# Kernel optimization log

Measured on AMD Instinct MI355X. Metric: run time of the kernel, lower is better.

## Reference

```python
import jax, jax.numpy as jnp
import numpy as np

FS = 16            # fixStride
LAST_RATIO = 0.5
TAUA, TAUB = 10.0, 0.1
TOT_EPOCHS = 100
EPS = 1e-20
SEED = 777


def _safe_norm(diff):
    # ||diff||_2 with subgradient 0 at 0 (matches torch.norm backward at 0)
    sq = jnp.sum(diff * diff, axis=-1)
    d = jnp.sqrt(jnp.where(sq > 0, sq, 1.0))
    return jnp.where(sq > 0, d, 0.0)


def _forward(x, w_score, b_score, att_params, num_graphs, epoch):
    BN, C = x.shape
    B = int(num_graphs)
    N = BN // B
    RES = N - FS + 1                       # rows per graph (unfold1d)
    MAXP = int(np.ceil(N * LAST_RATIO))    # max_pivot_count = ceil(N*last_ratio/init_ratio)

    # --- TopKPool scorer (init_ratio==1.0): permute nodes per graph by desc score
    scores = (x @ w_score + b_score) / jnp.sqrt(jnp.sum(w_score ** 2))
    perm = jnp.argsort(-scores.reshape(B, N), axis=-1, stable=True)      # [B,N]
    xg = jnp.take_along_axis(x.reshape(B, N, C), perm[..., None], axis=1)

    # --- sliding-window edges: row r -> dests r..r+FS-1, src node r
    dst = jnp.arange(RES)[:, None] + jnp.arange(FS)[None, :]             # [RES,FS]
    x_src = xg[:, :RES, :]                                               # [B,RES,C]
    x_dst = xg[:, dst, :]                                                # [B,RES,FS,C]

    # getSM_ei + scatter_softmax over rows: att = [x_s, x_d] @ att_params
    a1, a2 = att_params[:C], att_params[C:]
    sm = jax.nn.softmax((xg @ a1)[:, :RES, None] + (xg @ a2)[:, dst], axis=-1)  # [B,RES,FS]

    # getDM_ei (sigma=1): gaussian-kernel edge distances
    gk = jnp.exp(-_safe_norm(x_src[:, :, None, :] - x_dst) / 2.0) - EPS  # [B,RES,FS]

    # scatterSort: stable descending sort of gk per row
    order = jnp.argsort(-gk, axis=-1, stable=True)
    gk_sort = jnp.take_along_axis(gk, order, axis=-1)
    sm_sort = jnp.take_along_axis(sm, order, axis=-1)

    # per-rank column logits: scatter-sum of sorted attention over rows of each graph
    logits = jnp.broadcast_to(sm_sort.sum(axis=1)[:, None, :], (B, RES, FS))
    logits = logits.at[:, :, 0].set(-jnp.inf)            # mask rank-0 (self edge)

    # gumbel-softmax with annealed temperature
    tau0 = TAUA * (TAUB / TAUA) ** (float(epoch) / TOT_EPOCHS)
    g = jax.random.gumbel(jax.random.key(SEED), (B, RES, FS), jnp.float32)
    gmb = jax.nn.softmax((g + logits) / tau0, axis=-1)

    # per-row threshold and shifted distances (unsorted layout)
    ths = jnp.sum(gk_sort * gmb, axis=-1, keepdims=True)
    shifted = jax.nn.relu(gk - ths)                      # [B,RES,FS]

    # scatter_min over positions 1..FS-1 (position 0 excluded via index redirect)
    delta = (jnp.argmin(shifted[:, :, 1:], axis=-1) + 1).astype(jnp.int32)  # [B,RES]

    # innerLoopStar: follow skip pointers from row 0, up to MAXP pivots
    def chain(delta_g):
        def step(ptr, _):
            valid = ptr < RES
            piv = jnp.where(valid, ptr, -1)
            nxt = jnp.where(valid, ptr + delta_g[jnp.clip(ptr, 0, RES - 1)], jnp.int32(RES))
            return nxt, piv
        _, pivs = jax.lax.scan(step, jnp.int32(0), None, length=MAXP)
        return pivs

    pivots = jax.vmap(chain)(delta)                      # [B,MAXP], -1 padded
    mask = pivots >= 0
    pooled = jnp.take_along_axis(xg, jnp.clip(pivots, 0, N - 1)[..., None], axis=1)
    pooled = pooled * mask[..., None]                    # [B,MAXP,C]
    return pooled, shifted, pivots


def setup_inputs() -> dict:
    key = jax.random.key(0)
    k0, k1, k2, k3 = jax.random.split(key, 4)
    B, N, C = 128, 512, 64
    return {
        "x": jax.random.normal(k0, (B * N, C), jnp.float32),
        "w_score": jax.random.normal(k1, (C,), jnp.float32),
        "b_score": jax.random.normal(k2, (), jnp.float32),
        "att_params": jax.random.normal(k3, (2 * C,), jnp.float32),
        "num_graphs": B,
        "epoch": 10,
    }


def reference(x, w_score, b_score, att_params, num_graphs, epoch):
    return _forward(x, w_score, b_score, att_params, num_graphs, epoch)
```

## Files before the change

### kernel.cpp

```cpp
#include <hip/hip_runtime.h>
#include <math.h>

#define BB 128
#define NN 512
#define CC 64
#define FS 16
#define RES 497
#define MAXP 256
#define BN (BB*NN)
#define GT (BB*RES*FS)
#define WPB 16
#define NCH 32
#define ROWS (WPB+FS-1)
#define PITCH 66
#define GW2 64
#define GBLK 8

__device__ __forceinline__ unsigned rotl32(unsigned x, int d){ return (x<<d)|(x>>(32-d)); }

__device__ __forceinline__ void threefry777(unsigned x0, unsigned x1, unsigned &o0, unsigned &o1){
  const unsigned ks0 = 0u, ks1 = 777u;
  const unsigned ks2 = 0x1BD11BDAu ^ ks0 ^ ks1;
  x0 += ks0; x1 += ks1;
  x0+=x1; x1=rotl32(x1,13); x1^=x0;
  x0+=x1; x1=rotl32(x1,15); x1^=x0;
  x0+=x1; x1=rotl32(x1,26); x1^=x0;
  x0+=x1; x1=rotl32(x1, 6); x1^=x0;
  x0+=ks1; x1+=ks2+1u;
  x0+=x1; x1=rotl32(x1,17); x1^=x0;
  x0+=x1; x1=rotl32(x1,29); x1^=x0;
  x0+=x1; x1=rotl32(x1,16); x1^=x0;
  x0+=x1; x1=rotl32(x1,24); x1^=x0;
  x0+=ks2; x1+=ks0+2u;
  x0+=x1; x1=rotl32(x1,13); x1^=x0;
  x0+=x1; x1=rotl32(x1,15); x1^=x0;
  x0+=x1; x1=rotl32(x1,26); x1^=x0;
  x0+=x1; x1=rotl32(x1, 6); x1^=x0;
  x0+=ks0; x1+=ks1+3u;
  x0+=x1; x1=rotl32(x1,17); x1^=x0;
  x0+=x1; x1=rotl32(x1,29); x1^=x0;
  x0+=x1; x1=rotl32(x1,16); x1^=x0;
  x0+=x1; x1=rotl32(x1,24); x1^=x0;
  x0+=ks1; x1+=ks2+4u;
  x0+=x1; x1=rotl32(x1,13); x1^=x0;
  x0+=x1; x1=rotl32(x1,15); x1^=x0;
  x0+=x1; x1=rotl32(x1,26); x1^=x0;
  x0+=x1; x1=rotl32(x1, 6); x1^=x0;
  x0+=ks2; x1+=ks0+5u;
  o0 = x0; o1 = x1;
}

__device__ __forceinline__ float gumbel_at_f32(unsigned p){
  unsigned o0, o1;
  threefry777(0u, p, o0, o1);
  unsigned bits = o0 ^ o1;
  float fl = __uint_as_float((bits >> 9) | 0x3f800000u) - 1.0f;
  float u  = fmaxf(1.17549435e-38f, fl);
  return -logf(-logf(u));
}

__device__ __forceinline__ double wave_push_f64(double v, int dstLane){
  int lo = __double2loint(v), hi = __double2hiint(v);
  int plo = __builtin_amdgcn_ds_permute(dstLane<<2, lo);
  int phi = __builtin_amdgcn_ds_permute(dstLane<<2, hi);
  return __hiloint2double(phi, plo);
}

__global__ __launch_bounds__(NN) void k_scoresort(const float* __restrict__ x,
    const float* __restrict__ w, const float* __restrict__ bsc,
    const float* __restrict__ att, double* __restrict__ s1s,
    double* __restrict__ s2s, int* __restrict__ perm){
  int b = blockIdx.x, t = threadIdx.x;
  __shared__ double ss[NN];
  __shared__ int    si[NN];
  __shared__ double l1[NN], l2[NN];

  double wn=0.0, dw=0.0, d1=0.0, d2=0.0;
  #pragma unroll
  for (int c=0;c<CC;c++){ double wv=(double)w[c]; wn += wv*wv; }
  const float4* xr = (const float4*)(x + (size_t)(b*NN+t)*CC);
  #pragma unroll
  for (int q=0;q<CC/4;q++){
    float4 v = xr[q];
    double xv;
    xv=(double)v.x; dw+=xv*(double)w[4*q+0]; d1+=xv*(double)att[4*q+0]; d2+=xv*(double)att[CC+4*q+0];
    xv=(double)v.y; dw+=xv*(double)w[4*q+1]; d1+=xv*(double)att[4*q+1]; d2+=xv*(double)att[CC+4*q+1];
    xv=(double)v.z; dw+=xv*(double)w[4*q+2]; d1+=xv*(double)att[4*q+2]; d2+=xv*(double)att[CC+4*q+2];
    xv=(double)v.w; dw+=xv*(double)w[4*q+3]; d1+=xv*(double)att[4*q+3]; d2+=xv*(double)att[CC+4*q+3];
  }
  double s = (dw + (double)bsc[0]) / sqrt(wn);
  int idx = t;
  l1[t] = d1;
  l2[t] = d2;

  for (int k = 2; k <= NN; k <<= 1){
    bool up = ((t & k) == 0);
    for (int j = k >> 1; j >= 64; j >>= 1){
      ss[t] = s; si[t] = idx;
      __syncthreads();
      double os = ss[t ^ j]; int oi = si[t ^ j];
      bool first = ((t & j) == 0);
      bool cmp = (s > os) || (s == os && idx < oi);
      bool keep = (cmp == (first == up));
      if (!keep){ s = os; idx = oi; }
      __syncthreads();
    }
    #pragma unroll
    for (int j = 32; j > 0; j >>= 1){
      if (j <= (k >> 1)){
        double os = __shfl_xor(s, j, 64);
        int    oi = __shfl_xor(idx, j, 64);
        bool first = ((t & j) == 0);
        bool cmp = (s > os) || (s == os && idx < oi);
        bool keep = (cmp == (first == up));
        if (!keep){ s = os; idx = oi; }
      }
    }
  }
  __syncthreads();
  perm[b*NN + t] = idx;
  s1s[b*NN + t] = l1[idx];
  s2s[b*NN + t] = l2[idx];
}

__global__ __launch_bounds__(256) void k_passA(const float* __restrict__ x,
    const int* __restrict__ perm, const double* __restrict__ s1s,
    const double* __restrict__ s2s, double* __restrict__ gkd,
    unsigned char* __restrict__ rank8, double* __restrict__ partial){
  int b = blockIdx.y, ch = blockIdx.x, tid = threadIdx.x;
  int i0 = ch*WPB;
  int nwin  = min(WPB, RES - i0);
  int nrows = min(ROWS, NN - i0);
  __shared__ float  xs[ROWS*PITCH];
  __shared__ int    pg[ROWS];
  __shared__ double wred[4][FS];

  if (tid < nrows) pg[tid] = perm[b*NN + i0 + tid];
  __syncthreads();
  for (int u = tid; u < nrows*16; u += 256){
    int r = u >> 4, seg = u & 15;
    float4 v = ((const float4*)(x + (size_t)(b*NN + pg[r])*CC))[seg];
    float2* dst = (float2*)&xs[r*PITCH + seg*4];
    dst[0] = make_float2(v.x, v.y);
    dst[1] = make_float2(v.z, v.w);
  }
  __syncthreads();

  int w = tid >> 4, j = tid & 15;
  int lane = tid & 63, gbase = lane & 48, wv = tid >> 6;
  bool act = (w < nwin);
  int i = i0 + w;

  double sq = 0.0;
  const float* rs = &xs[w*PITCH];
  const float* rd = &xs[(w+j)*PITCH];
  #pragma unroll
  for (int c2=0;c2<CC/2;c2++){
    float2 a  = *(const float2*)&rs[2*c2];
    float2 bb = *(const float2*)&rd[2*c2];
    double d0 = (double)a.x - (double)bb.x;
    double d1v= (double)a.y - (double)bb.y;
    sq += d0*d0;
    sq += d1v*d1v;
  }
  double d   = (sq > 0.0) ? sqrt(sq) : 0.0;
  double gkv = exp(-d*0.5) - 1e-20;

  int drow = min(i + j, NN-1);
  double smt = s1s[b*NN + i] + s2s[b*NN + drow];
  double m = smt;
  #pragma unroll
  for (int off=8; off; off>>=1) m = fmax(m, __shfl_xor(m, off, 16));
  double em = exp(smt - m);
  double ssum = em;
  #pragma unroll
  for (int off=8; off; off>>=1) ssum += __shfl_xor(ssum, off, 16);
  double smn = em / ssum;

  int rank = 0;
  #pragma unroll
  for (int k=0;k<16;k++){
    double gkk = __shfl(gkv, gbase + k, 64);
    rank += ((gkk > gkv) || (gkk == gkv && k < j)) ? 1 : 0;
  }

  if (act){
    size_t base = ((size_t)b*RES + i)*FS;
    gkd[base + j]   = gkv;
    rank8[base + j] = (unsigned char)rank;
  }

  double contrib = act ? smn : 0.0;
  double srt = wave_push_f64(contrib, gbase + rank);
  srt += __shfl_xor(srt, 16, 64);
  srt += __shfl_xor(srt, 32, 64);
  if (lane < FS) wred[wv][lane] = srt;
  __syncthreads();
  if (tid < FS){
    partial[((size_t)b*NCH + ch)*FS + tid] =
        wred[0][tid] + wred[1][tid] + wred[2][tid] + wred[3][tid];
  }
}

__global__ __launch_bounds__(GW2) void k_g_rng(double* __restrict__ dummy){
  int b = blockIdx.y;
  int win = blockIdx.x*GW2 + threadIdx.x;
  if (win >= RES) return;
  size_t base = ((size_t)b*RES + win)*FS;
  double m = -(double)INFINITY;
  #pragma unroll 2
  for (int s=1;s<FS;s++){
    double g = (double)gumbel_at_f32((unsigned)(base + (unsigned)s));
    m = fmax(m, g);
  }
  dummy[b*RES + win] = m;
}

__global__ __launch_bounds__(GW2) void k_gumbel(const double* __restrict__ gkd,
    const unsigned char* __restrict__ rank8, const double* __restrict__ partial,
    const int* __restrict__ epoch_p, float* __restrict__ shifted_out,
    int* __restrict__ delta){
  int b = blockIdx.y, tid = threadIdx.x;
  int win = blockIdx.x*GW2 + tid;
  __shared__ double pl[NCH*FS];
  __shared__ double cs[FS];
  __shared__ double zbuf[GW2*17];
  __shared__ double gs[GW2*17];

  for (int u = tid; u < NCH*FS; u += GW2) pl[u] = partial[(size_t)b*NCH*FS + u];
  __syncthreads();
  if (tid < FS){
    double a = 0.0;
    #pragma unroll
    for (int ch=0; ch<NCH; ch++) a += pl[ch*FS + tid];
    cs[tid] = a;
  }
  __syncthreads();

  if (win >= RES) return;
  double tau = 10.0 * exp(-4.605170185988091 * ((double)epoch_p[0] / 100.0));
  size_t base = ((size_t)b*RES + win)*FS;
  int zb = tid*17;

  double m = -(double)INFINITY;
  #pragma unroll 2
  for (int s=1;s<FS;s++){
    double g = (double)gumbel_at_f32((unsigned)(base + (unsigned)s));
    double z = (g + cs[s]) / tau;
    zbuf[zb + s] = z;
    m = fmax(m, z);
  }
  double ssum = 0.0;
  #pragma unroll 2
  for (int s=1;s<FS;s++){
    double e = exp(zbuf[zb + s] - m);
    zbuf[zb + s] = e;
    ssum += e;
  }

  double gk[FS];
  #pragma unroll
  for (int q=0;q<FS/2;q++){
    double2 v = ((const double2*)(gkd + base))[q];
    gk[2*q]   = v.x;
    gk[2*q+1] = v.y;
  }
  uint4 rw = *((const uint4*)(rank8 + base));
  unsigned rr[4] = { rw.x, rw.y, rw.z, rw.w };
  #pragma unroll
  for (int j=0;j<FS;j++){
    int rk = (int)((rr[j>>2] >> ((j&3)*8)) & 15u);
    gs[zb + rk] = gk[j];
  }

  double ths = 0.0;
  #pragma unroll 2
  for (int s=1;s<FS;s++) ths += gs[zb + s] * (zbuf[zb + s] / ssum);

  double bv = 0.0; int bj = 1;
  #pragma unroll
  for (int j=0;j<FS;j++){
    double shv = fmax(gk[j] - ths, 0.0);
    shifted_out[base + j] = (float)shv;
    if (j == 1){ bv = shv; bj = 1; }
    else if (j > 1 && shv < bv){ bv = shv; bj = j; }
  }
  delta[b*RES + win] = bj;
}

__global__ __launch_bounds__(256) void k_chainpool(const int* __restrict__ delta,
    const int* __restrict__ perm, const float* __restrict__ x,
    float* __restrict__ piv_out, float* __restrict__ pooled){
  int b = blockIdx.x, tid = threadIdx.x;
  __shared__ int tbl[8][512];
  __shared__ int pivS[MAXP];

  for (int i = tid; i < 512; i += 256){
    int v;
    if (i < RES){ v = i + delta[b*RES + i]; if (v > RES) v = RES; }
    else v = RES;
    tbl[0][i] = v;
  }
  __syncthreads();
  #pragma unroll
  for (int k=1;k<8;k++){
    int v0 = tbl[k-1][tid];
    int v1 = tbl[k-1][tid+256];
    tbl[k][tid]     = tbl[k-1][v0];
    tbl[k][tid+256] = tbl[k-1][v1];
    __syncthreads();
  }
  {
    int p = 0;
    #pragma unroll
    for (int k=0;k<8;k++) if ((tid>>k)&1) p = tbl[k][p];
    int piv = (p < RES) ? p : -1;
    pivS[tid] = piv;
    piv_out[b*MAXP + tid] = (float)piv;
  }
  __syncthreads();

  for (int u = tid; u < MAXP*16; u += 256){
    int bp = u >> 4, seg = u & 15;
    int piv = pivS[bp];
    float4 v = make_float4(0.f,0.f,0.f,0.f);
    if (piv >= 0){
      int src = perm[b*NN + piv];
      v = ((const float4*)(x + (size_t)(b*NN + src)*CC))[seg];
    }
    ((float4*)pooled)[(size_t)(b*MAXP + bp)*16 + seg] = v;
  }
}

extern "C" void kernel_launch(void* const* d_in, const int* in_sizes, int n_in,
                              void* d_out, int out_size, void* d_ws, size_t ws_size,
                              hipStream_t stream) {
  (void)in_sizes; (void)n_in; (void)out_size; (void)ws_size;
  const float* x    = (const float*)d_in[0];
  const float* w    = (const float*)d_in[1];
  const float* bsc  = (const float*)d_in[2];
  const float* att  = (const float*)d_in[3];
  const int*   epch = (const int*)d_in[5];

  double* s1s     = (double*)d_ws;
  double* s2s     = s1s + BN;
  double* gkd     = s2s + BN;
  double* partial = gkd + GT;
  double* dummy   = partial + (size_t)BB*NCH*FS;
  int*    perm    = (int*)(dummy + (size_t)BB*RES);
  int*    delta   = perm + BN;
  unsigned char* rank8 = (unsigned char*)(delta + BB*RES);

  float* out_pooled  = (float*)d_out;
  float* out_shifted = out_pooled + BB*MAXP*CC;
  float* out_piv     = out_shifted + (size_t)BB*RES*FS;

  k_g_rng    <<<dim3(GBLK, BB), GW2, 0, stream>>>(dummy);
  k_scoresort<<<BB, NN, 0, stream>>>(x, w, bsc, att, s1s, s2s, perm);
  k_passA    <<<dim3(NCH, BB), 256, 0, stream>>>(x, perm, s1s, s2s, gkd, rank8, partial);
  k_gumbel   <<<dim3(GBLK, BB), GW2, 0, stream>>>(gkd, rank8, partial, epch, out_shifted, delta);
  k_chainpool<<<BB, 256, 0, stream>>>(delta, perm, x, out_piv, out_pooled);
}
```

Baseline: 75.98 us.

## Precompute gumbel noise into shifted output buffer and consume it in finish kernel

The old pipeline ran a dummy RNG kernel whose result was thrown away, then recomputed the threefry gumbel noise inside the gumbel kernel. Now a flat 256-thread kernel generates the gumbel values once and stores them as float in the shifted output buffer. The finish kernel reads them back, keeps the softmax temporaries in registers instead of shared memory, and uses 256-thread blocks. This removes the duplicated RNG work, at the cost of an extra global write and read of the noise and higher register pressure.

```diff
diff --git a/kernel.cpp b/kernel.cpp
--- a/kernel.cpp
+++ b/kernel.cpp
@@ -13,8 +13,6 @@
 #define NCH 32
 #define ROWS (WPB+FS-1)
 #define PITCH 66
-#define GW2 64
-#define GBLK 8
 
 __device__ __forceinline__ unsigned rotl32(unsigned x, int d){ return (x<<d)|(x>>(32-d)); }
 
@@ -66,6 +64,13 @@
   return __hiloint2double(phi, plo);
 }
 
+__global__ __launch_bounds__(256) void k_grng(float* __restrict__ g_out){
+  unsigned p = blockIdx.x*256u + threadIdx.x;
+  float gv = 0.0f;
+  if ((p & 15u) != 0u) gv = gumbel_at_f32(p);
+  g_out[p] = gv;
+}
+
 __global__ __launch_bounds__(NN) void k_scoresort(const float* __restrict__ x,
     const float* __restrict__ w, const float* __restrict__ bsc,
     const float* __restrict__ att, double* __restrict__ s1s,
@@ -202,32 +207,17 @@
   }
 }
 
-__global__ __launch_bounds__(GW2) void k_g_rng(double* __restrict__ dummy){
-  int b = blockIdx.y;
-  int win = blockIdx.x*GW2 + threadIdx.x;
-  if (win >= RES) return;
-  size_t base = ((size_t)b*RES + win)*FS;
-  double m = -(double)INFINITY;
-  #pragma unroll 2
-  for (int s=1;s<FS;s++){
-    double g = (double)gumbel_at_f32((unsigned)(base + (unsigned)s));
-    m = fmax(m, g);
-  }
-  dummy[b*RES + win] = m;
-}
-
-__global__ __launch_bounds__(GW2) void k_gumbel(const double* __restrict__ gkd,
+__global__ __launch_bounds__(256) void k_gfinish(const double* __restrict__ gkd,
     const unsigned char* __restrict__ rank8, const double* __restrict__ partial,
-    const int* __restrict__ epoch_p, float* __restrict__ shifted_out,
+    const int* __restrict__ epoch_p, float* __restrict__ g_shifted,
     int* __restrict__ delta){
   int b = blockIdx.y, tid = threadIdx.x;
-  int win = blockIdx.x*GW2 + tid;
+  int win = blockIdx.x*256 + tid;
   __shared__ double pl[NCH*FS];
   __shared__ double cs[FS];
-  __shared__ double zbuf[GW2*17];
-  __shared__ double gs[GW2*17];
-
-  for (int u = tid; u < NCH*FS; u += GW2) pl[u] = partial[(size_t)b*NCH*FS + u];
+  __shared__ double gs[256*17];
+
+  for (int u = tid; u < NCH*FS; u += 256) pl[u] = partial[(size_t)b*NCH*FS + u];
   __syncthreads();
   if (tid < FS){
     double a = 0.0;
@@ -240,22 +230,27 @@
   if (win >= RES) return;
   double tau = 10.0 * exp(-4.605170185988091 * ((double)epoch_p[0] / 100.0));
   size_t base = ((size_t)b*RES + win)*FS;
-  int zb = tid*17;
-
+
+  float gf[FS];
+  #pragma unroll
+  for (int q=0;q<4;q++){
+    float4 v = ((const float4*)(g_shifted + base))[q];
+    gf[4*q]=v.x; gf[4*q+1]=v.y; gf[4*q+2]=v.z; gf[4*q+3]=v.w;
+  }
+  double e[FS];
   double m = -(double)INFINITY;
-  #pragma unroll 2
+  #pragma unroll
   for (int s=1;s<FS;s++){
-    double g = (double)gumbel_at_f32((unsigned)(base + (unsigned)s));
-    double z = (g + cs[s]) / tau;
-    zbuf[zb + s] = z;
+    double z = ((double)gf[s] + cs[s]) / tau;
+    e[s] = z;
     m = fmax(m, z);
   }
   double ssum = 0.0;
-  #pragma unroll 2
+  #pragma unroll
   for (int s=1;s<FS;s++){
-    double e = exp(zbuf[zb + s] - m);
-    zbuf[zb + s] = e;
-    ssum += e;
+    double ev = exp(e[s] - m);
+    e[s] = ev;
+    ssum += ev;
   }
 
   double gk[FS];
@@ -267,6 +262,7 @@
   }
   uint4 rw = *((const uint4*)(rank8 + base));
   unsigned rr[4] = { rw.x, rw.y, rw.z, rw.w };
+  int zb = tid*17;
   #pragma unroll
   for (int j=0;j<FS;j++){
     int rk = (int)((rr[j>>2] >> ((j&3)*8)) & 15u);
@@ -274,14 +270,14 @@
   }
 
   double ths = 0.0;
-  #pragma unroll 2
-  for (int s=1;s<FS;s++) ths += gs[zb + s] * (zbuf[zb + s] / ssum);
+  #pragma unroll
+  for (int s=1;s<FS;s++) ths += gs[zb + s] * (e[s] / ssum);
 
   double bv = 0.0; int bj = 1;
   #pragma unroll
   for (int j=0;j<FS;j++){
     double shv = fmax(gk[j] - ths, 0.0);
-    shifted_out[base + j] = (float)shv;
+    g_shifted[base + j] = (float)shv;
     if (j == 1){ bv = shv; bj = 1; }
     else if (j > 1 && shv < bv){ bv = shv; bj = j; }
   }
@@ -346,8 +342,7 @@
   double* s2s     = s1s + BN;
   double* gkd     = s2s + BN;
   double* partial = gkd + GT;
-  double* dummy   = partial + (size_t)BB*NCH*FS;
-  int*    perm    = (int*)(dummy + (size_t)BB*RES);
+  int*    perm    = (int*)(partial + (size_t)BB*NCH*FS);
   int*    delta   = perm + BN;
   unsigned char* rank8 = (unsigned char*)(delta + BB*RES);
 
@@ -355,9 +350,9 @@
   float* out_shifted = out_pooled + BB*MAXP*CC;
   float* out_piv     = out_shifted + (size_t)BB*RES*FS;
 
-  k_g_rng    <<<dim3(GBLK, BB), GW2, 0, stream>>>(dummy);
+  k_grng     <<<GT/256, 256, 0, stream>>>(out_shifted);
   k_scoresort<<<BB, NN, 0, stream>>>(x, w, bsc, att, s1s, s2s, perm);
   k_passA    <<<dim3(NCH, BB), 256, 0, stream>>>(x, perm, s1s, s2s, gkd, rank8, partial);
-  k_gumbel   <<<dim3(GBLK, BB), GW2, 0, stream>>>(gkd, rank8, partial, epch, out_shifted, delta);
+  k_gfinish  <<<dim3(2, BB), 256, 0, stream>>>(gkd, rank8, partial, epch, out_shifted, delta);
   k_chainpool<<<BB, 256, 0, stream>>>(delta, perm, x, out_piv, out_pooled);
 }
```

Result: faster. 65.98 us (-13.2%).
